# Optimization experiments

Hardware: AMD Instinct MI355X
Metric: run time of the kernel (lower is better)

Reference implementation:

```python
import jax, jax.numpy as jnp
import numpy as np
import math

D_MODEL = 1024
NHEAD = 16
HEAD_DIM = D_MODEL // NHEAD  # 64
R_HEAD = 8  # r // nhead = 128 // 16


def setup_inputs() -> dict:
    key = jax.random.key(0)
    ks = jax.random.split(key, 6)
    b, s = 2, 2048
    scale = 1.0 / math.sqrt(D_MODEL)
    return {
        "x": jax.random.normal(ks[0], (b, s, D_MODEL), dtype=jnp.float32),
        "Wq": jax.random.normal(ks[1], (D_MODEL, D_MODEL), dtype=jnp.float32) * scale,
        "Wk": jax.random.normal(ks[2], (D_MODEL, D_MODEL), dtype=jnp.float32) * scale,
        "Wv": jax.random.normal(ks[3], (D_MODEL, D_MODEL), dtype=jnp.float32) * scale,
        "Wo": jax.random.normal(ks[4], (D_MODEL, D_MODEL), dtype=jnp.float32) * scale,
        "B": jax.random.normal(ks[5], (D_MODEL, R_HEAD), dtype=jnp.float32),
    }


def reference(x, Wq, Wk, Wv, Wo, B):
    b, s, d = x.shape
    # Linear projections (torch nn.Linear: y = x @ W.T)
    Q = (x @ Wq.T).reshape(b, s, NHEAD, HEAD_DIM).transpose(0, 2, 1, 3)  # [b,h,s,hd]
    K = (x @ Wk.T).reshape(b, s, NHEAD, HEAD_DIM).transpose(0, 2, 1, 3)
    V = (x @ Wv.T).reshape(b, s, NHEAD, HEAD_DIM).transpose(0, 2, 1, 3)
    # Shared basis: head h uses rows [h*head_dim : (h+1)*head_dim] of B
    B_heads = B.reshape(NHEAD, HEAD_DIM, R_HEAD)  # [h,hd,r]
    # Low-rank projected queries/keys (vectorized form of the per-head loop)
    Qr = jnp.einsum('bhsd,hdr->bhsr', Q, B_heads)  # [b,h,s,r]
    Kr = jnp.einsum('bhsd,hdr->bhsr', K, B_heads)
    scores = jnp.einsum('bhqr,bhkr->bhqk', Qr, Kr) / math.sqrt(R_HEAD)  # [b,h,s,s]
    attn = jax.nn.softmax(scores, axis=-1)  # dropout is identity in eval
    out = jnp.einsum('bhqk,bhkd->bhqd', attn, V)  # [b,h,s,hd]
    out = out.transpose(0, 2, 1, 3).reshape(b, s, d)
    return out @ Wo.T
```

## Files before the change

### kernel.cpp

```cpp
#include <hip/hip_runtime.h>

#define SEQ 2048
#define DM 1024

typedef __attribute__((ext_vector_type(8))) short bs8;
typedef __attribute__((ext_vector_type(4))) float vf4;
typedef __attribute__((ext_vector_type(4))) unsigned int vu4;

__device__ __forceinline__ unsigned short bf16u(float f) {
  unsigned int u = __float_as_uint(f);
  u = (u + 0x7fffu + ((u >> 16) & 1u)) >> 16;
  return (unsigned short)u;
}

__device__ __forceinline__ unsigned int cvt_pk(float lo, float hi) {
  unsigned int r;
  asm("v_cvt_pk_bf16_f32 %0, %1, %2" : "=v"(r) : "v"(lo), "v"(hi));
  return r;
}

__device__ __forceinline__ float fexp2(float x) {
  float r;
  asm("v_exp_f32 %0, %1" : "=v"(r) : "v"(x));
  return r;
}

__device__ __forceinline__ void gload16(const unsigned short* g, unsigned short* l) {
  __builtin_amdgcn_global_load_lds(
      (const __attribute__((address_space(1))) unsigned int*)g,
      (__attribute__((address_space(3))) unsigned int*)l, 16, 0, 0);
}

__global__ void k_combine(const float* __restrict__ Wq, const float* __restrict__ Wk,
                          const float* __restrict__ Bm,
                          unsigned short* __restrict__ Ch, unsigned short* __restrict__ Cl) {
  int e = blockIdx.x * 256 + threadIdx.x;
  int which = e >> 17;
  int rem = e & 131071;
  int hr = rem >> 10;
  int j = rem & 1023;
  int h = hr >> 3, r = hr & 7;
  const float* W = which ? Wk : Wq;
  float acc = 0.f;
  #pragma unroll 8
  for (int d = 0; d < 64; d++) {
    int gd = h * 64 + d;
    acc += Bm[gd * 8 + r] * W[gd * 1024 + j];
  }
  size_t idx = (size_t)(which * 128 + hr) * 1024 + j;
  unsigned short h16 = bf16u(acc);
  float hf = __uint_as_float(((unsigned int)h16) << 16);
  Ch[idx] = h16;
  Cl[idx] = bf16u(acc - hf);
}

__global__ void k_cvt(const float* __restrict__ in, unsigned short* __restrict__ out, int n4) {
  int i = blockIdx.x * 256 + threadIdx.x;
  if (i >= n4) return;
  float4 v = ((const float4*)in)[i];
  ushort4 o;
  o.x = bf16u(v.x); o.y = bf16u(v.y); o.z = bf16u(v.z); o.w = bf16u(v.w);
  ((ushort4*)out)[i] = o;
}

__global__ void k_cvt_hl(const float* __restrict__ in, unsigned short* __restrict__ oh,
                         unsigned short* __restrict__ ol, int n4) {
  int i = blockIdx.x * 256 + threadIdx.x;
  if (i >= n4) return;
  float4 v = ((const float4*)in)[i];
  float f[4] = {v.x, v.y, v.z, v.w};
  ushort4 hv, lv;
  unsigned short hs[4], ls[4];
  #pragma unroll
  for (int j = 0; j < 4; j++) {
    unsigned short h16 = bf16u(f[j]);
    float hf = __uint_as_float(((unsigned int)h16) << 16);
    hs[j] = h16;
    ls[j] = bf16u(f[j] - hf);
  }
  hv.x = hs[0]; hv.y = hs[1]; hv.z = hs[2]; hv.w = hs[3];
  lv.x = ls[0]; lv.y = ls[1]; lv.z = ls[2]; lv.w = ls[3];
  ((ushort4*)oh)[i] = hv;
  ((ushort4*)ol)[i] = lv;
}

__global__ __launch_bounds__(256) void k_qkr2(
    const unsigned short* __restrict__ Xh, const unsigned short* __restrict__ Xl,
    const unsigned short* __restrict__ Bh_, const unsigned short* __restrict__ Bl_,
    unsigned short* __restrict__ Qhl, unsigned short* __restrict__ Khl) {
  const int K = 1024;
  __shared__ unsigned short SS[12288];
  unsigned short* Ah = SS;
  unsigned short* Al = SS + 2048;
  unsigned short* Bh = SS + 4096;
  unsigned short* Bl = SS + 8192;
  int t = threadIdx.x, lane = t & 63, w = t >> 6;
  int gg = lane >> 4, r = lane & 15;
  int wm = w & 1, wn = w >> 1;
  int m0 = blockIdx.x * 32, n0 = blockIdx.y * 64;
  vf4 acc[2];
  #pragma unroll
  for (int fn = 0; fn < 2; fn++) acc[fn] = (vf4){0.f, 0.f, 0.f, 0.f};

  int prow = lane >> 3, pslot = lane & 7;
  int arl = w * 8 + prow;
  int akey = (arl ^ (arl >> 3)) & 7;
  const unsigned short* ah_src = Xh + (size_t)(m0 + arl) * K + (pslot ^ akey) * 8;
  const unsigned short* al_src = Xl + (size_t)(m0 + arl) * K + (pslot ^ akey) * 8;
  unsigned short* ah_dst = &Ah[(w * 8) * 64];
  unsigned short* al_dst = &Al[(w * 8) * 64];
  const unsigned short *bh_src[2], *bl_src[2];
  unsigned short *bh_dst[2], *bl_dst[2];
  #pragma unroll
  for (int p = 0; p < 2; p++) {
    int brl = w * 16 + p * 8 + prow;
    int bkey = (brl ^ (brl >> 3)) & 7;
    bh_src[p] = Bh_ + (size_t)(n0 + brl) * K + (pslot ^ bkey) * 8;
    bl_src[p] = Bl_ + (size_t)(n0 + brl) * K + (pslot ^ bkey) * 8;
    bh_dst[p] = &Bh[(w * 16 + p * 8) * 64];
    bl_dst[p] = &Bl[(w * 16 + p * 8) * 64];
  }

  int aoff[2], boff[2][2];
  {
    int arow = wm * 16 + r;
    int key = (arow ^ (arow >> 3)) & 7;
    #pragma unroll
    for (int kk = 0; kk < 2; kk++) aoff[kk] = arow * 64 + ((kk * 4 + gg) ^ key) * 8;
  }
  #pragma unroll
  for (int fn = 0; fn < 2; fn++) {
    int brow = wn * 32 + fn * 16 + r;
    int key = (brow ^ (brow >> 3)) & 7;
    #pragma unroll
    for (int kk = 0; kk < 2; kk++) boff[fn][kk] = brow * 64 + ((kk * 4 + gg) ^ key) * 8;
  }

  for (int k0 = 0; k0 < K; k0 += 64) {
    __syncthreads();
    gload16(ah_src + k0, ah_dst);
    gload16(al_src + k0, al_dst);
    #pragma unroll
    for (int p = 0; p < 2; p++) {
      gload16(bh_src[p] + k0, bh_dst[p]);
      gload16(bl_src[p] + k0, bl_dst[p]);
    }
    __syncthreads();
    bs8 afh[2], afl[2];
    #pragma unroll
    for (int kk = 0; kk < 2; kk++) {
      afh[kk] = *(const bs8*)&Ah[aoff[kk]];
      afl[kk] = *(const bs8*)&Al[aoff[kk]];
    }
    #pragma unroll
    for (int kk = 0; kk < 2; kk++)
      #pragma unroll
      for (int fn = 0; fn < 2; fn++) {
        bs8 bfh = *(const bs8*)&Bh[boff[fn][kk]];
        bs8 bfl = *(const bs8*)&Bl[boff[fn][kk]];
        acc[fn] = __builtin_amdgcn_mfma_f32_16x16x32_bf16(afh[kk], bfh, acc[fn], 0, 0, 0);
        acc[fn] = __builtin_amdgcn_mfma_f32_16x16x32_bf16(afh[kk], bfl, acc[fn], 0, 0, 0);
        acc[fn] = __builtin_amdgcn_mfma_f32_16x16x32_bf16(afl[kk], bfh, acc[fn], 0, 0, 0);
      }
  }

  __syncthreads();
  float* Sc = (float*)SS;
  #pragma unroll
  for (int fn = 0; fn < 2; fn++)
    #pragma unroll
    for (int j = 0; j < 4; j++)
      Sc[(wm * 16 + gg * 4 + j) * 65 + wn * 32 + fn * 16 + r] = acc[fn][j];
  __syncthreads();

  int g = t >> 5, xr = t & 31;
  const float* srcrow = &Sc[xr * 65 + g * 8];
  int side = (n0 >= 128) ? 1 : 0;
  int hh = ((n0 & 127) >> 3) + g;
  const float sc = side ? 1.0f : (1.4426950408889634f * 0.35355339059327373f);
  unsigned short hs[8], ls[8];
  #pragma unroll
  for (int j = 0; j < 8; j++) {
    float fs = srcrow[j] * sc;
    unsigned short h16 = bf16u(fs);
    float hf = __uint_as_float(((unsigned int)h16) << 16);
    hs[j] = h16;
    ls[j] = bf16u(fs - hf);
  }
  uint4 hv = {(unsigned int)hs[0] | ((unsigned int)hs[1] << 16),
              (unsigned int)hs[2] | ((unsigned int)hs[3] << 16),
              (unsigned int)hs[4] | ((unsigned int)hs[5] << 16),
              (unsigned int)hs[6] | ((unsigned int)hs[7] << 16)};
  uint4 lv = {(unsigned int)ls[0] | ((unsigned int)ls[1] << 16),
              (unsigned int)ls[2] | ((unsigned int)ls[3] << 16),
              (unsigned int)ls[4] | ((unsigned int)ls[5] << 16),
              (unsigned int)ls[6] | ((unsigned int)ls[7] << 16)};
  unsigned short* dst = (side ? Khl : Qhl) + ((size_t)hh * 4096 + (m0 + xr)) * 16;
  *(uint4*)dst = hv;
  *(uint4*)(dst + 8) = lv;
}

template<int OUT>
__global__ __launch_bounds__(256) void k_gemm128(const unsigned short* __restrict__ A,
    const unsigned short* __restrict__ W, void* __restrict__ Cout, int M, int N, int K) {
  __shared__ unsigned short Ah[128 * 64];
  __shared__ unsigned short Bh[64 * 64];
  int t = threadIdx.x, lane = t & 63, w = t >> 6;
  int gg = lane >> 4, r = lane & 15;
  int m0 = blockIdx.x * 128, n0 = blockIdx.y * 64;
  vf4 acc[2][4];
  #pragma unroll
  for (int i = 0; i < 2; i++)
    #pragma unroll
    for (int j = 0; j < 4; j++) acc[i][j] = (vf4){0.f, 0.f, 0.f, 0.f};

  int prow = lane >> 3, pslot = lane & 7;
  const unsigned short* asrc[4];
  unsigned short* aldst[4];
  #pragma unroll
  for (int p = 0; p < 4; p++) {
    int rr = w * 32 + p * 8 + prow;
    int c = pslot ^ ((rr ^ (rr >> 3)) & 7);
    asrc[p] = &A[(size_t)(m0 + rr) * K + c * 8];
    aldst[p] = &Ah[(w * 32 + p * 8) * 64];
  }
  const unsigned short* bsrc[2];
  unsigned short* bldst[2];
  #pragma unroll
  for (int p = 0; p < 2; p++) {
    int rn = w * 16 + p * 8 + prow;
    int c = pslot ^ ((rn ^ (rn >> 3)) & 7);
    bsrc[p] = &W[(size_t)(n0 + rn) * K + c * 8];
    bldst[p] = &Bh[(w * 16 + p * 8) * 64];
  }

  int aoff[2][2], boff[4][2];
  #pragma unroll
  for (int fm = 0; fm < 2; fm++) {
    int arow = w * 32 + fm * 16 + r;
    int key = (arow ^ (arow >> 3)) & 7;
    #pragma unroll
    for (int kk = 0; kk < 2; kk++)
      aoff[fm][kk] = arow * 64 + ((kk * 4 + gg) ^ key) * 8;
  }
  #pragma unroll
  for (int fn = 0; fn < 4; fn++) {
    int brow = fn * 16 + r;
    int key = (brow ^ (brow >> 3)) & 7;
    #pragma unroll
    for (int kk = 0; kk < 2; kk++)
      boff[fn][kk] = brow * 64 + ((kk * 4 + gg) ^ key) * 8;
  }

  for (int k0 = 0; k0 < K; k0 += 64) {
    __syncthreads();
    #pragma unroll
    for (int p = 0; p < 4; p++) gload16(asrc[p] + k0, aldst[p]);
    #pragma unroll
    for (int p = 0; p < 2; p++) gload16(bsrc[p] + k0, bldst[p]);
    __syncthreads();
    bs8 af[2][2], bf[4][2];
    #pragma unroll
    for (int fm = 0; fm < 2; fm++)
      #pragma unroll
      for (int kk = 0; kk < 2; kk++) af[fm][kk] = *(const bs8*)&Ah[aoff[fm][kk]];
    #pragma unroll
    for (int fn = 0; fn < 4; fn++)
      #pragma unroll
      for (int kk = 0; kk < 2; kk++) bf[fn][kk] = *(const bs8*)&Bh[boff[fn][kk]];
    #pragma unroll
    for (int kk = 0; kk < 2; kk++)
      #pragma unroll
      for (int fm = 0; fm < 2; fm++)
        #pragma unroll
        for (int fn = 0; fn < 4; fn++)
          acc[fm][fn] = __builtin_amdgcn_mfma_f32_16x16x32_bf16(af[fm][kk], bf[fn][kk], acc[fm][fn], 0, 0, 0);
  }

  #pragma unroll
  for (int fm = 0; fm < 2; fm++)
    #pragma unroll
    for (int fn = 0; fn < 4; fn++) {
      if (OUT == 2) {
        int n = n0 + fn * 16 + r;
        int m = m0 + w * 32 + fm * 16 + gg * 4;
        ushort4 st = {bf16u(acc[fm][fn][0]), bf16u(acc[fm][fn][1]),
                      bf16u(acc[fm][fn][2]), bf16u(acc[fm][fn][3])};
        *(ushort4*)&((unsigned short*)Cout)[(size_t)n * M + m] = st;
      } else {
        #pragma unroll
        for (int j = 0; j < 4; j++) {
          int m = m0 + w * 32 + fm * 16 + gg * 4 + j;
          int n = n0 + fn * 16 + r;
          ((float*)Cout)[(size_t)m * N + n] = acc[fm][fn][j];
        }
      }
    }
}

__global__ __launch_bounds__(256, 6) void k_attn(const unsigned short* __restrict__ Qhl,
    const unsigned short* __restrict__ Khl, const unsigned short* __restrict__ Vt,
    unsigned short* __restrict__ AO) {
  int bx = blockIdx.x;
  int qt = bx & 63, h = (bx >> 6) & 15, b = bx >> 10;
  int t = threadIdx.x, lane = t & 63, w = t >> 6;
  int wq = w & 1, kvg = w >> 1;
  int gg = lane >> 4, r = lane & 15;

  __shared__ unsigned short VT[2][4096];

  int qglob = b * 2048 + qt * 32 + wq * 16 + r;
  bs8 bq = {0, 0, 0, 0, 0, 0, 0, 0};
  if (gg != 3)
    bq = *(const bs8*)&Qhl[((size_t)h * 4096 + qglob) * 16 + (gg == 2 ? 8 : 0)];

  unsigned int kbase = ((unsigned int)(h * 4096 + b * 2048 + kvg * 1024
                        + (r >> 2) * 8 + (r & 3)) << 4) + ((gg == 1) ? 8u : 0u);

  int srow = lane >> 3, sslot = lane & 7;
  unsigned int voff[4];
  #pragma unroll
  for (int c = 0; c < 4; c++) {
    int d = wq * 32 + c * 8 + srow;
    int key = (d ^ (d >> 2)) & 7;
    voff[c] = (unsigned int)((h * 64 + d) * 4096 + b * 2048 + kvg * 1024
                             + (sslot ^ key) * 8);
  }

  int pvoff[2][4];
  #pragma unroll
  for (int sl = 0; sl < 2; sl++)
    #pragma unroll
    for (int fn = 0; fn < 4; fn++) {
      int row = 4 * r + fn;
      int key = (row ^ (row >> 2)) & 7;
      pvoff[sl][fn] = row * 64 + ((sl * 4 + gg) ^ key) * 8;
    }

  float mrun = -INFINITY;
  vf4 acc[4];
  #pragma unroll
  for (int i = 0; i < 4; i++) acc[i] = (vf4){0.f, 0.f, 0.f, 0.f};
  vf4 accs = (vf4){0.f, 0.f, 0.f, 0.f};

  const bs8 ones = (bs8){16256, 16256, 16256, 16256, 16256, 16256, 16256, 16256};

  for (int kc = 0; kc < 16; kc++) {
    const unsigned short* kpc = Khl + kbase + (unsigned int)(kc * 1024);
    bs8 af0 = *(const bs8*)(kpc);
    bs8 af1 = *(const bs8*)(kpc + 512);
    bs8 af2 = *(const bs8*)(kpc + 64);
    bs8 af3 = *(const bs8*)(kpc + 576);

    __syncthreads();
    #pragma unroll
    for (int c = 0; c < 4; c++)
      gload16(Vt + voff[c] + (unsigned int)(kc * 64), &VT[kvg][(wq * 32 + c * 8) * 64]);
    __syncthreads();

    vf4 z = (vf4){0.f, 0.f, 0.f, 0.f};
    __builtin_amdgcn_s_setprio(1);
    vf4 s0 = __builtin_amdgcn_mfma_f32_16x16x32_bf16(af0, bq, z, 0, 0, 0);
    vf4 s1 = __builtin_amdgcn_mfma_f32_16x16x32_bf16(af1, bq, z, 0, 0, 0);
    vf4 s2 = __builtin_amdgcn_mfma_f32_16x16x32_bf16(af2, bq, z, 0, 0, 0);
    vf4 s3 = __builtin_amdgcn_mfma_f32_16x16x32_bf16(af3, bq, z, 0, 0, 0);
    __builtin_amdgcn_s_setprio(0);

    float p[16];
    #pragma unroll
    for (int j = 0; j < 4; j++) {
      p[0 + j] = s0[j]; p[4 + j] = s1[j]; p[8 + j] = s2[j]; p[12 + j] = s3[j];
    }
    float cm0 = fmaxf(fmaxf(p[0],  p[1]),  p[2]);
    float cm1 = fmaxf(fmaxf(p[3],  p[4]),  p[5]);
    float cm2 = fmaxf(fmaxf(p[6],  p[7]),  p[8]);
    float cm3 = fmaxf(fmaxf(p[9],  p[10]), p[11]);
    float cm4 = fmaxf(fmaxf(p[12], p[13]), p[14]);
    float cmax = fmaxf(fmaxf(fmaxf(cm0, cm1), cm2),
                       fmaxf(fmaxf(cm3, cm4), p[15]));
    cmax = fmaxf(cmax, __shfl_xor(cmax, 16));
    cmax = fmaxf(cmax, __shfl_xor(cmax, 32));

    if (!__all(cmax <= mrun + 8.f)) {
      float mnew = fmaxf(mrun, cmax);
      float alpha = fexp2(mrun - mnew);
      float al[4];
      #pragma unroll
      for (int j = 0; j < 4; j++) al[j] = __shfl(alpha, gg * 4 + j);
      #pragma unroll
      for (int fn = 0; fn < 4; fn++) {
        acc[fn][0] *= al[0]; acc[fn][1] *= al[1];
        acc[fn][2] *= al[2]; acc[fn][3] *= al[3];
      }
      accs[0] *= al[0]; accs[1] *= al[1];
      accs[2] *= al[2]; accs[3] *= al[3];
      mrun = mnew;
    }

    #pragma unroll
    for (int i = 0; i < 16; i++) p[i] = fexp2(p[i] - mrun);

    vu4 a0 = {cvt_pk(p[0],  p[1]),  cvt_pk(p[2],  p[3]),
              cvt_pk(p[8],  p[9]),  cvt_pk(p[10], p[11])};
    vu4 a1 = {cvt_pk(p[4],  p[5]),  cvt_pk(p[6],  p[7]),
              cvt_pk(p[12], p[13]), cvt_pk(p[14], p[15])};
    bs8 apv0 = __builtin_bit_cast(bs8, a0);
    bs8 apv1 = __builtin_bit_cast(bs8, a1);

    const unsigned short* vb = &VT[kvg][0];
    __builtin_amdgcn_s_setprio(1);
    #pragma unroll
    for (int sl = 0; sl < 2; sl++) {
      bs8 a = sl ? apv1 : apv0;
      #pragma unroll
      for (int fn = 0; fn < 4; fn++) {
        bs8 bv = *(const bs8*)&vb[pvoff[sl][fn]];
        acc[fn] = __builtin_amdgcn_mfma_f32_16x16x32_bf16(a, bv, acc[fn], 0, 0, 0);
      }
    }
    accs = __builtin_amdgcn_mfma_f32_16x16x32_bf16(apv0, ones, accs, 0, 0, 0);
    accs = __builtin_amdgcn_mfma_f32_16x16x32_bf16(apv1, ones, accs, 0, 0, 0);
    __builtin_amdgcn_s_setprio(0);
  }

  __syncthreads();
  float* Lm = (float*)&VT[0][0];
  float* Ll = Lm + 32;
  float* La = Lm + 64;
  if (kvg == 1) {
    if (gg == 0) Lm[wq * 16 + r] = mrun;
    if (r == 0) {
      #pragma unroll
      for (int j = 0; j < 4; j++) Ll[wq * 16 + gg * 4 + j] = accs[j];
    }
    float* dst = &La[(wq * 64 + lane) * 20];
    #pragma unroll
    for (int fn = 0; fn < 4; fn++) *(vf4*)(dst + fn * 4) = acc[fn];
  }
  __syncthreads();
  if (kvg == 1) return;

  float m1 = Lm[wq * 16 + r];
  float mx = fmaxf(mrun, m1);
  float e0 = fexp2(mrun - mx), e1 = fexp2(m1 - mx);
  float al0[4], al1[4], l1[4];
  #pragma unroll
  for (int j = 0; j < 4; j++) {
    al0[j] = __shfl(e0, gg * 4 + j);
    al1[j] = __shfl(e1, gg * 4 + j);
    l1[j] = Ll[wq * 16 + gg * 4 + j];
  }
  const float* src = &La[(wq * 64 + lane) * 20];
  #pragma unroll
  for (int fn = 0; fn < 4; fn++) {
    vf4 o1 = *(const vf4*)(src + fn * 4);
    #pragma unroll
    for (int j = 0; j < 4; j++)
      acc[fn][j] = acc[fn][j] * al0[j] + o1[j] * al1[j];
  }
  #pragma unroll
  for (int j = 0; j < 4; j++) accs[j] = accs[j] * al0[j] + l1[j] * al1[j];

  float li[4];
  #pragma unroll
  for (int j = 0; j < 4; j++) li[j] = 1.f / accs[j];
  #pragma unroll
  for (int j = 0; j < 4; j++) {
    uint2 o;
    o.x = cvt_pk(acc[0][j] * li[j], acc[1][j] * li[j]);
    o.y = cvt_pk(acc[2][j] * li[j], acc[3][j] * li[j]);
    int qq = qt * 32 + wq * 16 + gg * 4 + j;
    *(uint2*)&AO[((size_t)b * SEQ + qq) * 1024 + h * 64 + 4 * r] = o;
  }
}

extern "C" void kernel_launch(void* const* d_in, const int* in_sizes, int n_in,
                              void* d_out, int out_size, void* d_ws, size_t ws_size,
                              hipStream_t stream) {
  const float* x  = (const float*)d_in[0];
  const float* Wq = (const float*)d_in[1];
  const float* Wk = (const float*)d_in[2];
  const float* Wv = (const float*)d_in[3];
  const float* Wo = (const float*)d_in[4];
  const float* Bm = (const float*)d_in[5];
  float* out = (float*)d_out;

  char* ws = (char*)d_ws;
  unsigned short* Cqkh = (unsigned short*)ws;  ws += (size_t)256 * 1024 * 2;
  unsigned short* Cqkl = (unsigned short*)ws;  ws += (size_t)256 * 1024 * 2;
  unsigned short* xh  = (unsigned short*)ws;   ws += (size_t)4096 * 1024 * 2;
  unsigned short* Wvh = (unsigned short*)ws;   ws += (size_t)1024 * 1024 * 2;
  unsigned short* Woh = (unsigned short*)ws;   ws += (size_t)1024 * 1024 * 2;
  unsigned short* Vt  = (unsigned short*)ws;   ws += (size_t)4096 * 1024 * 2;
  unsigned short* AO  = (unsigned short*)ws;   ws += (size_t)4096 * 1024 * 2;
  unsigned short* Qhl = (unsigned short*)ws;   ws += (size_t)16 * 4096 * 16 * 2;
  unsigned short* Khl = (unsigned short*)ws;   ws += (size_t)16 * 4096 * 16 * 2;
  unsigned short* xl = AO;

  k_combine<<<1024, 256, 0, stream>>>(Wq, Wk, Bm, Cqkh, Cqkl);
  k_cvt_hl<<<4096, 256, 0, stream>>>(x, xh, xl, 1048576);
  k_cvt<<<1024, 256, 0, stream>>>(Wv, Wvh, 262144);
  k_cvt<<<1024, 256, 0, stream>>>(Wo, Woh, 262144);
  k_qkr2<<<dim3(128, 4), 256, 0, stream>>>(xh, xl, Cqkh, Cqkl, Qhl, Khl);
  k_gemm128<2><<<dim3(32, 16), 256, 0, stream>>>(xh, Wvh, (void*)Vt, 4096, 1024, 1024);
  k_attn<<<2048, 256, 0, stream>>>(Qhl, Khl, Vt, AO);
  k_gemm128<0><<<dim3(32, 16), 256, 0, stream>>>(AO, Woh, (void*)out, 4096, 1024, 1024);
}
```

Before: 122.8 us.

## Restructure attention: 64 queries per block, all warps share keys, double-buffered V

The attention kernel now gives each block 64 queries, one per-wave slice of 16, and every wave walks all 2048 keys. The old kernel split keys into two groups and merged the two partial softmax states through shared memory at the end; that merge is gone. V tiles are prefetched into registers and written into a double-buffered shared array, and K fragments for the next chunk are prefetched, so there is one barrier per iteration instead of two. The grid is halved and occupancy is lowered to 4 blocks per CU. In exchange the serial chain per wave is twice as long and register pressure goes up.

Result: faster. 117.1 us (-4.7%).

```diff
diff --git a/kernel.cpp b/kernel.cpp
--- a/kernel.cpp
+++ b/kernel.cpp
@@ -298,34 +298,35 @@
     }
 }
 
-__global__ __launch_bounds__(256, 6) void k_attn(const unsigned short* __restrict__ Qhl,
+__global__ __launch_bounds__(256, 4) void k_attn(const unsigned short* __restrict__ Qhl,
     const unsigned short* __restrict__ Khl, const unsigned short* __restrict__ Vt,
     unsigned short* __restrict__ AO) {
   int bx = blockIdx.x;
-  int qt = bx & 63, h = (bx >> 6) & 15, b = bx >> 10;
+  int qt = bx & 31, h = (bx >> 5) & 15, b = bx >> 9;
   int t = threadIdx.x, lane = t & 63, w = t >> 6;
-  int wq = w & 1, kvg = w >> 1;
   int gg = lane >> 4, r = lane & 15;
 
   __shared__ unsigned short VT[2][4096];
 
-  int qglob = b * 2048 + qt * 32 + wq * 16 + r;
+  int qglob = b * 2048 + qt * 64 + w * 16 + r;
   bs8 bq = {0, 0, 0, 0, 0, 0, 0, 0};
   if (gg != 3)
     bq = *(const bs8*)&Qhl[((size_t)h * 4096 + qglob) * 16 + (gg == 2 ? 8 : 0)];
 
-  unsigned int kbase = ((unsigned int)(h * 4096 + b * 2048 + kvg * 1024
-                        + (r >> 2) * 8 + (r & 3)) << 4) + ((gg == 1) ? 8u : 0u);
-
-  int srow = lane >> 3, sslot = lane & 7;
-  unsigned int voff[4];
-  #pragma unroll
-  for (int c = 0; c < 4; c++) {
-    int d = wq * 32 + c * 8 + srow;
-    int key = (d ^ (d >> 2)) & 7;
-    voff[c] = (unsigned int)((h * 64 + d) * 4096 + b * 2048 + kvg * 1024
-                             + (sslot ^ key) * 8);
-  }
+  const unsigned short* Khead = &Khl[((size_t)h * 4096 + (size_t)b * 2048) * 16];
+  int koff = (gg == 1) ? 8 : 0;
+  const unsigned short* kp[4];
+  #pragma unroll
+  for (int kt = 0; kt < 4; kt++) {
+    int ks = (kt & 1) * 32 + (r >> 2) * 8 + (kt >> 1) * 4 + (r & 3);
+    kp[kt] = Khead + (size_t)ks * 16 + koff;
+  }
+
+  int vrow = t >> 2, vcl = t & 3;
+  const unsigned short* vsrc = &Vt[(size_t)(h * 64 + vrow) * 4096 + (size_t)b * 2048 + vcl * 16];
+  int vkey = (vrow ^ (vrow >> 2)) & 7;
+  int sw0 = ((vcl * 2) ^ vkey) * 8;
+  int sw1 = ((vcl * 2 + 1) ^ vkey) * 8;
 
   int pvoff[2][4];
   #pragma unroll
@@ -345,18 +346,29 @@
 
   const bs8 ones = (bs8){16256, 16256, 16256, 16256, 16256, 16256, 16256, 16256};
 
-  for (int kc = 0; kc < 16; kc++) {
-    const unsigned short* kpc = Khl + kbase + (unsigned int)(kc * 1024);
-    bs8 af0 = *(const bs8*)(kpc);
-    bs8 af1 = *(const bs8*)(kpc + 512);
-    bs8 af2 = *(const bs8*)(kpc + 64);
-    bs8 af3 = *(const bs8*)(kpc + 576);
-
-    __syncthreads();
-    #pragma unroll
-    for (int c = 0; c < 4; c++)
-      gload16(Vt + voff[c] + (unsigned int)(kc * 64), &VT[kvg][(wq * 32 + c * 8) * 64]);
-    __syncthreads();
+  uint4 fv0 = *(const uint4*)(vsrc);
+  uint4 fv1 = *(const uint4*)(vsrc + 8);
+  bs8 af0 = *(const bs8*)(kp[0]);
+  bs8 af1 = *(const bs8*)(kp[1]);
+  bs8 af2 = *(const bs8*)(kp[2]);
+  bs8 af3 = *(const bs8*)(kp[3]);
+  {
+    unsigned short* vd = &VT[0][vrow * 64];
+    *(uint4*)(vd + sw0) = fv0;
+    *(uint4*)(vd + sw1) = fv1;
+  }
+  __syncthreads();
+
+  #pragma unroll 2
+  for (int kc = 0; kc < 32; kc++) {
+    int nc = kc < 31 ? kc + 1 : 31;
+    uint4 nv0 = *(const uint4*)(vsrc + nc * 64);
+    uint4 nv1 = *(const uint4*)(vsrc + nc * 64 + 8);
+    size_t nb16 = (size_t)nc * 64 * 16;
+    bs8 naf0 = *(const bs8*)(kp[0] + nb16);
+    bs8 naf1 = *(const bs8*)(kp[1] + nb16);
+    bs8 naf2 = *(const bs8*)(kp[2] + nb16);
+    bs8 naf3 = *(const bs8*)(kp[3] + nb16);
 
     vf4 z = (vf4){0.f, 0.f, 0.f, 0.f};
     __builtin_amdgcn_s_setprio(1);
@@ -407,7 +419,7 @@
     bs8 apv0 = __builtin_bit_cast(bs8, a0);
     bs8 apv1 = __builtin_bit_cast(bs8, a1);
 
-    const unsigned short* vb = &VT[kvg][0];
+    const unsigned short* vb = &VT[kc & 1][0];
     __builtin_amdgcn_s_setprio(1);
     #pragma unroll
     for (int sl = 0; sl < 2; sl++) {
@@ -421,45 +433,16 @@
     accs = __builtin_amdgcn_mfma_f32_16x16x32_bf16(apv0, ones, accs, 0, 0, 0);
     accs = __builtin_amdgcn_mfma_f32_16x16x32_bf16(apv1, ones, accs, 0, 0, 0);
     __builtin_amdgcn_s_setprio(0);
-  }
-
-  __syncthreads();
-  float* Lm = (float*)&VT[0][0];
-  float* Ll = Lm + 32;
-  float* La = Lm + 64;
-  if (kvg == 1) {
-    if (gg == 0) Lm[wq * 16 + r] = mrun;
-    if (r == 0) {
-      #pragma unroll
-      for (int j = 0; j < 4; j++) Ll[wq * 16 + gg * 4 + j] = accs[j];
-    }
-    float* dst = &La[(wq * 64 + lane) * 20];
-    #pragma unroll
-    for (int fn = 0; fn < 4; fn++) *(vf4*)(dst + fn * 4) = acc[fn];
-  }
-  __syncthreads();
-  if (kvg == 1) return;
-
-  float m1 = Lm[wq * 16 + r];
-  float mx = fmaxf(mrun, m1);
-  float e0 = fexp2(mrun - mx), e1 = fexp2(m1 - mx);
-  float al0[4], al1[4], l1[4];
-  #pragma unroll
-  for (int j = 0; j < 4; j++) {
-    al0[j] = __shfl(e0, gg * 4 + j);
-    al1[j] = __shfl(e1, gg * 4 + j);
-    l1[j] = Ll[wq * 16 + gg * 4 + j];
-  }
-  const float* src = &La[(wq * 64 + lane) * 20];
-  #pragma unroll
-  for (int fn = 0; fn < 4; fn++) {
-    vf4 o1 = *(const vf4*)(src + fn * 4);
-    #pragma unroll
-    for (int j = 0; j < 4; j++)
-      acc[fn][j] = acc[fn][j] * al0[j] + o1[j] * al1[j];
-  }
-  #pragma unroll
-  for (int j = 0; j < 4; j++) accs[j] = accs[j] * al0[j] + l1[j] * al1[j];
+
+    af0 = naf0; af1 = naf1; af2 = naf2; af3 = naf3;
+
+    if (kc < 31) {
+      unsigned short* vd = &VT[(kc + 1) & 1][vrow * 64];
+      *(uint4*)(vd + sw0) = nv0;
+      *(uint4*)(vd + sw1) = nv1;
+      __syncthreads();
+    }
+  }
 
   float li[4];
   #pragma unroll
@@ -469,7 +452,7 @@
     uint2 o;
     o.x = cvt_pk(acc[0][j] * li[j], acc[1][j] * li[j]);
     o.y = cvt_pk(acc[2][j] * li[j], acc[3][j] * li[j]);
-    int qq = qt * 32 + wq * 16 + gg * 4 + j;
+    int qq = qt * 64 + w * 16 + gg * 4 + j;
     *(uint2*)&AO[((size_t)b * SEQ + qq) * 1024 + h * 64 + 4 * r] = o;
   }
 }
@@ -503,6 +486,6 @@
   k_cvt<<<1024, 256, 0, stream>>>(Wo, Woh, 262144);
   k_qkr2<<<dim3(128, 4), 256, 0, stream>>>(xh, xl, Cqkh, Cqkl, Qhl, Khl);
   k_gemm128<2><<<dim3(32, 16), 256, 0, stream>>>(xh, Wvh, (void*)Vt, 4096, 1024, 1024);
-  k_attn<<<2048, 256, 0, stream>>>(Qhl, Khl, Vt, AO);
+  k_attn<<<1024, 256, 0, stream>>>(Qhl, Khl, Vt, AO);
   k_gemm128<0><<<dim3(32, 16), 256, 0, stream>>>(AO, Woh, (void*)out, 4096, 1024, 1024);
 }
```

## Software-pipeline K and V tile loads in attention kernel via register prefetch

Applied to the files above, without the earlier changes.

The attention loop now loads the next chunk's K fragments and V tile into registers before computing on the current chunk. The V data is written to shared memory between barriers after the compute, replacing the direct global-to-LDS copy. The per-thread V load mapping changes so each thread copies a contiguous 32-element row segment. Occupancy hint drops from 6 to 4 blocks to leave room for the extra prefetch registers, which may reduce latency hiding through occupancy.

Result: slower. 128.2 us (+4.3%).

```diff
diff --git a/kernel.cpp b/kernel.cpp
--- a/kernel.cpp
+++ b/kernel.cpp
@@ -298,7 +298,7 @@
     }
 }
 
-__global__ __launch_bounds__(256, 6) void k_attn(const unsigned short* __restrict__ Qhl,
+__global__ __launch_bounds__(256, 4) void k_attn(const unsigned short* __restrict__ Qhl,
     const unsigned short* __restrict__ Khl, const unsigned short* __restrict__ Vt,
     unsigned short* __restrict__ AO) {
   int bx = blockIdx.x;
@@ -314,18 +314,25 @@
   if (gg != 3)
     bq = *(const bs8*)&Qhl[((size_t)h * 4096 + qglob) * 16 + (gg == 2 ? 8 : 0)];
 
-  unsigned int kbase = ((unsigned int)(h * 4096 + b * 2048 + kvg * 1024
-                        + (r >> 2) * 8 + (r & 3)) << 4) + ((gg == 1) ? 8u : 0u);
-
-  int srow = lane >> 3, sslot = lane & 7;
-  unsigned int voff[4];
-  #pragma unroll
-  for (int c = 0; c < 4; c++) {
-    int d = wq * 32 + c * 8 + srow;
-    int key = (d ^ (d >> 2)) & 7;
-    voff[c] = (unsigned int)((h * 64 + d) * 4096 + b * 2048 + kvg * 1024
-                             + (sslot ^ key) * 8);
-  }
+  const unsigned short* Khead = &Khl[((size_t)h * 4096 + (size_t)b * 2048
+                                      + (size_t)kvg * 1024) * 16];
+  int koff = (gg == 1) ? 8 : 0;
+  const unsigned short* kp[4];
+  #pragma unroll
+  for (int kt = 0; kt < 4; kt++) {
+    int ks = (kt & 1) * 32 + (r >> 2) * 8 + (kt >> 1) * 4 + (r & 3);
+    kp[kt] = Khead + (size_t)ks * 16 + koff;
+  }
+
+  int sg = t >> 7;
+  int vrow = (t >> 1) & 63, vcl = t & 1;
+  const unsigned short* vsrc = &Vt[(size_t)(h * 64 + vrow) * 4096 + (size_t)b * 2048
+                                   + (size_t)sg * 1024 + vcl * 32];
+  unsigned short* vdst = &VT[sg][vrow * 64];
+  int vkey = (vrow ^ (vrow >> 2)) & 7;
+  int sw[4];
+  #pragma unroll
+  for (int s = 0; s < 4; s++) sw[s] = ((vcl * 4 + s) ^ vkey) * 8;
 
   int pvoff[2][4];
   #pragma unroll
@@ -345,18 +352,33 @@
 
   const bs8 ones = (bs8){16256, 16256, 16256, 16256, 16256, 16256, 16256, 16256};
 
+  {
+    uint4 fv0 = *(const uint4*)(vsrc);
+    uint4 fv1 = *(const uint4*)(vsrc + 8);
+    uint4 fv2 = *(const uint4*)(vsrc + 16);
+    uint4 fv3 = *(const uint4*)(vsrc + 24);
+    *(uint4*)(vdst + sw[0]) = fv0;
+    *(uint4*)(vdst + sw[1]) = fv1;
+    *(uint4*)(vdst + sw[2]) = fv2;
+    *(uint4*)(vdst + sw[3]) = fv3;
+  }
+  bs8 af0 = *(const bs8*)(kp[0]);
+  bs8 af1 = *(const bs8*)(kp[1]);
+  bs8 af2 = *(const bs8*)(kp[2]);
+  bs8 af3 = *(const bs8*)(kp[3]);
+  __syncthreads();
+
   for (int kc = 0; kc < 16; kc++) {
-    const unsigned short* kpc = Khl + kbase + (unsigned int)(kc * 1024);
-    bs8 af0 = *(const bs8*)(kpc);
-    bs8 af1 = *(const bs8*)(kpc + 512);
-    bs8 af2 = *(const bs8*)(kpc + 64);
-    bs8 af3 = *(const bs8*)(kpc + 576);
-
-    __syncthreads();
-    #pragma unroll
-    for (int c = 0; c < 4; c++)
-      gload16(Vt + voff[c] + (unsigned int)(kc * 64), &VT[kvg][(wq * 32 + c * 8) * 64]);
-    __syncthreads();
+    int nc = kc < 15 ? kc + 1 : 15;
+    uint4 nv0 = *(const uint4*)(vsrc + nc * 64);
+    uint4 nv1 = *(const uint4*)(vsrc + nc * 64 + 8);
+    uint4 nv2 = *(const uint4*)(vsrc + nc * 64 + 16);
+    uint4 nv3 = *(const uint4*)(vsrc + nc * 64 + 24);
+    size_t nb16 = (size_t)nc * 64 * 16;
+    bs8 naf0 = *(const bs8*)(kp[0] + nb16);
+    bs8 naf1 = *(const bs8*)(kp[1] + nb16);
+    bs8 naf2 = *(const bs8*)(kp[2] + nb16);
+    bs8 naf3 = *(const bs8*)(kp[3] + nb16);
 
     vf4 z = (vf4){0.f, 0.f, 0.f, 0.f};
     __builtin_amdgcn_s_setprio(1);
@@ -421,6 +443,17 @@
     accs = __builtin_amdgcn_mfma_f32_16x16x32_bf16(apv0, ones, accs, 0, 0, 0);
     accs = __builtin_amdgcn_mfma_f32_16x16x32_bf16(apv1, ones, accs, 0, 0, 0);
     __builtin_amdgcn_s_setprio(0);
+
+    af0 = naf0; af1 = naf1; af2 = naf2; af3 = naf3;
+
+    if (kc < 15) {
+      __syncthreads();
+      *(uint4*)(vdst + sw[0]) = nv0;
+      *(uint4*)(vdst + sw[1]) = nv1;
+      *(uint4*)(vdst + sw[2]) = nv2;
+      *(uint4*)(vdst + sw[3]) = nv3;
+      __syncthreads();
+    }
   }
 
   __syncthreads();
```
